# Performance work log

Hardware: AMD Instinct MI355X
Metric: run time of the kernel (lower is better)

Reference implementation:

```python
import jax, jax.numpy as jnp
import numpy as np

V = 256        # vocab (bytes)
DM = 1024      # d_model
NL = 8         # num layers
N = 16         # d_state
K = 4          # d_conv
E = 2 * DM     # d_inner (expand=2)
R = DM // 16   # dt_rank = 64
EPS = 1e-5
B, T = 1, 1024


def setup_inputs() -> dict:
    key = jax.random.key(0)
    ks = jax.random.split(key, 10)
    s = lambda i, shape, scale=0.02: jax.random.normal(ks[i], shape, jnp.float32) * scale
    A_init = jnp.log(jnp.tile(jnp.arange(1, N + 1, dtype=jnp.float32), (NL, E, 1)))
    return {
        "input_ids": jax.random.randint(ks[0], (B, T), 0, V),
        "embed": s(1, (V, DM)),
        "Wxz": s(2, (NL, DM, 2 * E)),            # in_proj (no bias)
        "conv_w": s(3, (NL, E, K), 0.1),          # depthwise causal conv
        "conv_b": jnp.zeros((NL, E), jnp.float32),
        "Wx": s(4, (NL, E, R + 2 * N)),           # x_proj -> dt, B, C
        "Wdt": s(5, (NL, R, E), 0.1),             # dt_proj
        "dt_bias": jnp.full((NL, E), -4.6, jnp.float32),  # softplus(-4.6) ~ 0.01
        "A_log": A_init,                          # A = -exp(A_log), S4D-real init
        "D": jnp.ones((NL, E), jnp.float32),      # skip connection
        "Wout": s(6, (NL, E, DM)),                # out_proj (no bias)
        "norm_w": jnp.ones((NL, DM), jnp.float32),
        "final_norm_w": jnp.ones((DM,), jnp.float32),
        "lm_head_w": s(7, (DM, V)),               # lm_head (no bias)
    }


def rmsnorm(x, w):
    return x * jax.lax.rsqrt(jnp.mean(x * x, axis=-1, keepdims=True) + EPS) * w


def selective_scan(x, dt, A, Bm, Cm, Dp):
    # x, dt: [B,T,E]; A: [E,N]; Bm, Cm: [B,T,N]; Dp: [E]
    dA = jnp.exp(dt[..., None] * A)                              # [B,T,E,N]
    dBx = dt[..., None] * Bm[:, :, None, :] * x[..., None]       # [B,T,E,N]

    def step(h, inp):
        dA_t, dBx_t, C_t = inp                                   # [B,E,N],[B,E,N],[B,N]
        h = dA_t * h + dBx_t
        y = jnp.einsum('ben,bn->be', h, C_t)
        return h, y

    h0 = jnp.zeros((x.shape[0], E, N), x.dtype)
    _, ys = jax.lax.scan(step, h0, (dA.transpose(1, 0, 2, 3),
                                    dBx.transpose(1, 0, 2, 3),
                                    Cm.transpose(1, 0, 2)))
    return ys.transpose(1, 0, 2) + Dp * x                        # [B,T,E]


def mamba_layer(h, p):
    Wxz, cw, cb, Wx, Wdt, dtb, A_log, Dp, Wout, nw = p
    res = h
    u = rmsnorm(h, nw)
    xz = u @ Wxz                                                 # [B,T,2E]
    x, z = jnp.split(xz, 2, axis=-1)
    # causal depthwise conv over time
    xc = jax.lax.conv_general_dilated(x.transpose(0, 2, 1), cw[:, None, :],
                                      (1,), [(K - 1, 0)], feature_group_count=E)
    x = jax.nn.silu(xc.transpose(0, 2, 1) + cb)                  # [B,T,E]
    xdbl = x @ Wx                                                # [B,T,R+2N]
    dt = jax.nn.softplus(xdbl[..., :R] @ Wdt + dtb)              # [B,T,E]
    Bm = xdbl[..., R:R + N]
    Cm = xdbl[..., R + N:]
    A = -jnp.exp(A_log)                                          # [E,N]
    y = selective_scan(x, dt, A, Bm, Cm, Dp)
    y = y * jax.nn.silu(z)
    return res + y @ Wout, None


def reference(input_ids, embed, Wxz, conv_w, conv_b, Wx, Wdt, dt_bias, A_log, D,
              Wout, norm_w, final_norm_w, lm_head_w):
    h = embed[input_ids]                                         # [B,T,DM]
    h, _ = jax.lax.scan(mamba_layer, h,
                        (Wxz, conv_w, conv_b, Wx, Wdt, dt_bias, A_log, D, Wout, norm_w))
    h = rmsnorm(h, final_norm_w)
    return h @ lm_head_w                                         # logits [B,T,V]
```

## Files before the change

### kernel.cpp

```cpp
#include <hip/hip_runtime.h>
#include <hip/hip_bf16.h>

#define DM_   1024
#define NLAY  8
#define NST   16
#define EE    2048
#define E2    4096
#define RNK   64
#define SEQ   1024
#define NXD   96
#define VOC   256
#define EPS_  1e-5f
#define NCH   32
#define CLEN  32
#define NTHR  256

typedef __attribute__((ext_vector_type(8))) short bf16x8;
typedef __attribute__((ext_vector_type(4))) float f32x4;
typedef __hip_bfloat16 bf16;

__device__ __forceinline__ float sigmoidf_(float x){ return 1.f/(1.f+__expf(-x)); }
__device__ __forceinline__ float softplusf_(float x){ return (x>15.f)?x:log1pf(__expf(x)); }
__device__ __forceinline__ short f2bf_s(float x){
  union { bf16 b; short s; } cv; cv.b = __float2bfloat16(x); return cv.s;
}

__device__ __forceinline__ void gld_lds16(const short* g, short* lds_uniform){
  __builtin_amdgcn_global_load_lds(
      (const __attribute__((address_space(1))) unsigned int*)(const void*)g,
      (__attribute__((address_space(3))) unsigned int*)(void*)lds_uniform,
      16, 0, 0);
}

__device__ void t_job(const float* in, bf16* out, int R, int C, int L, char* smem, int gdim){
  float (*tile)[33] = (float(*)[33])smem;
  int tC = C >> 5, tR = R >> 5;
  int per = tC * tR, total = per * L;
  int tx = threadIdx.x & 31, ty = threadIdx.x >> 5;
  for (int it = blockIdx.x; it < total; it += gdim){
    int l = it / per, rem = it - l*per;
    int tc = rem % tC, tr = rem / tC;
    const float* inp = in + (size_t)l*R*C;
    bf16* outp = out + (size_t)l*R*C;
    int c0 = tc*32, r0 = tr*32;
    __syncthreads();
#pragma unroll
    for (int j = 0; j < 4; j++)
      tile[ty + j*8][tx] = inp[(size_t)(r0+ty+j*8)*C + c0+tx];
    __syncthreads();
#pragma unroll
    for (int j = 0; j < 4; j++)
      outp[(size_t)(c0+ty+j*8)*R + r0+tx] = __float2bfloat16(tile[tx][ty+j*8]);
  }
}

__global__ __launch_bounds__(256) void k_prep(
    const float* __restrict__ Wxz, const float* __restrict__ Wout,
    const float* __restrict__ Wx, const float* __restrict__ Wdt,
    const float* __restrict__ lmw,
    bf16* wxz_bf, bf16* wout_bf, bf16* wx_bf, bf16* wdt_bf, bf16* lm_bf){
  __shared__ __align__(16) char smem[4352];
  int gdim = gridDim.x;
  t_job(Wxz,  wxz_bf,  DM_, E2,  NLAY, smem, gdim);
  t_job(Wout, wout_bf, EE,  DM_, NLAY, smem, gdim);
  t_job(Wx,   wx_bf,   EE,  NXD, NLAY, smem, gdim);
  t_job(Wdt,  wdt_bf,  RNK, EE,  NLAY, smem, gdim);
  t_job(lmw,  lm_bf,   DM_, VOC, 1,    smem, gdim);
}

__global__ void k_rmsnorm_fuse(const int* __restrict__ ids, const float* __restrict__ emb,
                               float* __restrict__ h, const float* __restrict__ s0,
                               const float* __restrict__ s1, const float* __restrict__ w,
                               bf16* __restrict__ u, float* __restrict__ zout){
  int t = blockIdx.x;
  float* hp = h + (size_t)t*DM_;
  float v[4];
  float ss = 0.f;
#pragma unroll
  for (int j = 0; j < 4; j++){
    int i = threadIdx.x + j*256;
    float x;
    if (ids){ x = emb[(size_t)ids[t]*DM_ + i]; hp[i] = x; }
    else { x = hp[i] + s0[(size_t)t*DM_ + i] + s1[(size_t)t*DM_ + i]; hp[i] = x; }
    v[j] = x; ss += x*x;
  }
#pragma unroll
  for (int o = 32; o > 0; o >>= 1) ss += __shfl_down(ss, o, 64);
  __shared__ float red[4];
  if ((threadIdx.x & 63) == 0) red[threadIdx.x >> 6] = ss;
  __syncthreads();
  float tot = red[0]+red[1]+red[2]+red[3];
  float sc = rsqrtf(tot*(1.f/DM_) + EPS_);
  bf16* up = u + (size_t)t*DM_;
#pragma unroll
  for (int j = 0; j < 4; j++){
    int i = threadIdx.x + j*256;
    up[i] = __float2bfloat16(v[j]*sc*w[i]);
  }
  if (zout) zout[(size_t)t*VOC + threadIdx.x] = 0.f;
}

template<int BM, int BN, int NWM, int NWN, int MODE>
__global__ __launch_bounds__(256) void k_gemm(
    const short* __restrict__ A, const short* __restrict__ Bt, float* __restrict__ C,
    int M, int N, int K, int Ksplit)
{
  constexpr int BK = 64;
  constexpr int WM = BM/NWM, WN = BN/NWN;
  constexpr int MT = WM/16, NT = WN/16;
  constexpr int ABY = BM*BK*2, BBY = BN*BK*2;
  constexpr int AISS = ABY/4096, BISS = BBY/4096;
  __shared__ __align__(16) short As[2][BM*BK];
  __shared__ __align__(16) short Bs[2][BN*BK];
  int tid = threadIdx.x, lane = tid & 63, wave = tid >> 6;
  int wr = wave / NWN, wc = wave % NWN;
  int m0 = blockIdx.x * BM, n0 = blockIdx.y * BN;
  int lrow = lane & 15, lq = lane >> 4;
  int wbase = (tid & ~63) * 16;

  int kbeg = blockIdx.z * Ksplit;
  int nk = Ksplit / BK;

  f32x4 acc[MT][NT];
#pragma unroll
  for (int i = 0; i < MT; i++)
#pragma unroll
    for (int j = 0; j < NT; j++) acc[i][j] = (f32x4){0.f,0.f,0.f,0.f};

  auto stage = [&](int k0, int buf){
#pragma unroll
    for (int i = 0; i < AISS; i++){
      int off = i*4096 + tid*16;
      int row = off >> 7;
      int kc  = ((off >> 4) & 7) ^ (row & 7);
      gld_lds16(A + (size_t)(m0+row)*K + k0 + kc*8, As[buf] + ((i*4096 + wbase) >> 1));
    }
#pragma unroll
    for (int i = 0; i < BISS; i++){
      int off = i*4096 + tid*16;
      int row = off >> 7;
      int kc  = ((off >> 4) & 7) ^ (row & 7);
      gld_lds16(Bt + (size_t)(n0+row)*K + k0 + kc*8, Bs[buf] + ((i*4096 + wbase) >> 1));
    }
  };

  stage(kbeg, 0);
  __syncthreads();
  for (int it = 0; it < nk; it++){
    int cur = it & 1;
    if (it + 1 < nk) stage(kbeg + (it+1)*BK, cur ^ 1);
#pragma unroll
    for (int s = 0; s < 2; s++){
      bf16x8 af[MT], bfr[NT];
#pragma unroll
      for (int mt = 0; mt < MT; mt++){
        int row = wr*WM + mt*16 + lrow;
        int cc = (s*4 + lq) ^ (row & 7);
        af[mt] = *(const bf16x8*)(As[cur] + row*BK + cc*8);
      }
#pragma unroll
      for (int nt = 0; nt < NT; nt++){
        int row = wc*WN + nt*16 + lrow;
        int cc = (s*4 + lq) ^ (row & 7);
        bfr[nt] = *(const bf16x8*)(Bs[cur] + row*BK + cc*8);
      }
#pragma unroll
      for (int mt = 0; mt < MT; mt++)
#pragma unroll
        for (int nt = 0; nt < NT; nt++)
          acc[mt][nt] = __builtin_amdgcn_mfma_f32_16x16x32_bf16(af[mt], bfr[nt], acc[mt][nt], 0,0,0);
    }
    __syncthreads();
  }

  size_t slab = (MODE == 4) ? (size_t)blockIdx.z * M * N : 0;
#pragma unroll
  for (int mt = 0; mt < MT; mt++){
    int row = m0 + wr*WM + mt*16 + lq*4;
#pragma unroll
    for (int nt = 0; nt < NT; nt++){
      int col = n0 + wc*WN + nt*16 + lrow;
#pragma unroll
      for (int r = 0; r < 4; r++){
        float v = acc[mt][nt][r];
        size_t idx = slab + (size_t)(row + r)*N + col;
        if (MODE == 5) atomicAdd(&C[idx], v);
        else C[idx] = v;
      }
    }
  }
}

__global__ void k_conv_silu(const float* __restrict__ xz, const float* __restrict__ cw,
                            const float* __restrict__ cb, float* __restrict__ xact,
                            bf16* __restrict__ xbf, float* __restrict__ xdbl){
  int t = blockIdx.y;
  int e = blockIdx.x*256 + threadIdx.x;
  float4 w4 = *(const float4*)(cw + (size_t)e*4);
  float acc = cb[e];
  if (t >= 3){
    acc += xz[(size_t)(t-3)*E2 + e]*w4.x + xz[(size_t)(t-2)*E2 + e]*w4.y
         + xz[(size_t)(t-1)*E2 + e]*w4.z + xz[(size_t)t*E2 + e]*w4.w;
  } else {
    const float* wp = (const float*)&w4;
#pragma unroll
    for (int k = 0; k < 4; k++){ int tt = t-3+k; if (tt >= 0) acc += xz[(size_t)tt*E2 + e]*wp[k]; }
  }
  float xv = acc * sigmoidf_(acc);
  size_t id = (size_t)t*EE + e;
  xact[id] = xv;
  xbf[id] = __float2bfloat16(xv);
  if (id < SEQ*NXD) xdbl[id] = 0.f;
}

__global__ __launch_bounds__(256) void k_dt_scanA(
    const float* __restrict__ xdbl, const short* __restrict__ WdtT,
    const float* __restrict__ dtb, const float* __restrict__ Alog,
    const float* __restrict__ xact, float* __restrict__ dtbuf,
    float* __restrict__ S, float* __restrict__ dtsum)
{
  __shared__ __align__(16) char smem[22528];
  short* As = (short*)smem;
  short* Bs = (short*)(smem + 8192);
  float (*dts)[65]  = (float(*)[65])smem;
  float (*Bcol)[17] = (float(*)[17])(smem + 16640);
  int tid = threadIdx.x;
  int lane = tid & 63, wave = tid >> 6;
  int wr = wave >> 1, wc = wave & 1, lrow = lane & 15, lq = lane >> 4;
  int m0 = blockIdx.x*64, n0 = blockIdx.y*64;

  {
    int row = tid >> 2;
    int kq  = (tid & 3) << 4;
    const float* src = xdbl + (size_t)(m0+row)*NXD + kq;
    short tmp[16] __attribute__((aligned(16)));
#pragma unroll
    for (int j = 0; j < 16; j++) tmp[j] = f2bf_s(src[j]);
    int c0 = ((kq>>3) + 0) ^ (row & 7);
    int c1 = ((kq>>3) + 1) ^ (row & 7);
    *(bf16x8*)(As + row*64 + c0*8) = *(const bf16x8*)(tmp);
    *(bf16x8*)(As + row*64 + c1*8) = *(const bf16x8*)(tmp + 8);
  }
  {
    int wbase = (tid & ~63) * 16;
#pragma unroll
    for (int i = 0; i < 2; i++){
      int off = i*4096 + tid*16;
      int row = off >> 7;
      int kc  = ((off >> 4) & 7) ^ (row & 7);
      gld_lds16(WdtT + (size_t)(n0+row)*RNK + kc*8, Bs + ((i*4096 + wbase) >> 1));
    }
  }
  __syncthreads();
  f32x4 acc[2][2];
#pragma unroll
  for (int i = 0; i < 2; i++)
#pragma unroll
    for (int j = 0; j < 2; j++) acc[i][j] = (f32x4){0.f,0.f,0.f,0.f};
#pragma unroll
  for (int s = 0; s < 2; s++){
    bf16x8 af[2], bfr[2];
#pragma unroll
    for (int mt = 0; mt < 2; mt++){
      int row = wr*32 + mt*16 + lrow;
      int cc = (s*4 + lq) ^ (row & 7);
      af[mt] = *(const bf16x8*)(As + row*64 + cc*8);
    }
#pragma unroll
    for (int nt = 0; nt < 2; nt++){
      int row = wc*32 + nt*16 + lrow;
      int cc = (s*4 + lq) ^ (row & 7);
      bfr[nt] = *(const bf16x8*)(Bs + row*64 + cc*8);
    }
#pragma unroll
    for (int mt = 0; mt < 2; mt++)
#pragma unroll
      for (int nt = 0; nt < 2; nt++)
        acc[mt][nt] = __builtin_amdgcn_mfma_f32_16x16x32_bf16(af[mt], bfr[nt], acc[mt][nt], 0,0,0);
  }
  __syncthreads();

#pragma unroll
  for (int mt = 0; mt < 2; mt++){
    int rl = wr*32 + mt*16 + lq*4;
#pragma unroll
    for (int nt = 0; nt < 2; nt++){
      int cl = wc*32 + nt*16 + lrow;
#pragma unroll
      for (int r = 0; r < 4; r++){
        float v = softplusf_(acc[mt][nt][r] + dtb[n0 + cl]);
        dtbuf[(size_t)(m0 + rl + r)*EE + n0 + cl] = v;
        dts[rl + r][cl] = v;
      }
    }
  }
  {
    int row = tid >> 2, n4 = (tid & 3) << 2;
    float4 b4 = *(const float4*)(xdbl + (size_t)(m0+row)*NXD + RNK + n4);
    Bcol[row][n4+0] = b4.x; Bcol[row][n4+1] = b4.y;
    Bcol[row][n4+2] = b4.z; Bcol[row][n4+3] = b4.w;
  }
  __syncthreads();

  if (tid < 128){
    int ch = tid >> 6, el = tid & 63;
    int e = n0 + el;
    int c = (m0 >> 5) + ch;
    int t0 = c*CLEN;
    const float* Al = Alog + (size_t)e*NST;
    float Ae[NST];
#pragma unroll
    for (int n = 0; n < NST; n++) Ae[n] = -__expf(Al[n]);
    float h[NST];
#pragma unroll
    for (int n = 0; n < NST; n++) h[n] = 0.f;
    float ds = 0.f;
    for (int tt = 0; tt < CLEN; tt++){
      float dtv = dts[ch*CLEN + tt][el];
      float xv  = xact[(size_t)(t0+tt)*EE + e];
      ds += dtv;
      float sx = dtv*xv;
#pragma unroll
      for (int n = 0; n < NST; n++)
        h[n] = __expf(dtv*Ae[n])*h[n] + sx*Bcol[ch*CLEN + tt][n];
    }
    float* Sp = S + ((size_t)c*EE + e)*NST;
#pragma unroll
    for (int n = 0; n < NST; n++) Sp[n] = h[n];
    dtsum[(size_t)c*EE + e] = ds;
  }
}

__global__ void k_scanC(const float* __restrict__ dt, const float* __restrict__ x,
                        const float* __restrict__ xdbl, const float* __restrict__ Alog,
                        const float* __restrict__ Dp, const float* __restrict__ S,
                        const float* __restrict__ dtsum, const float* __restrict__ xz,
                        bf16* __restrict__ ybf){
  int e = blockIdx.x*256 + threadIdx.x;
  int c = blockIdx.y;
  int t0 = c*CLEN;
  float Ae[NST];
#pragma unroll
  for (int n = 0; n < NST; n++) Ae[n] = -__expf(Alog[(size_t)e*NST + n]);
  __shared__ float Bsm[CLEN][NST], Csm[CLEN][NST];
  for (int i = threadIdx.x; i < CLEN*NST; i += 256){
    int tt = i>>4, n = i&15;
    Bsm[tt][n] = xdbl[(size_t)(t0+tt)*NXD + RNK + n];
    Csm[tt][n] = xdbl[(size_t)(t0+tt)*NXD + RNK + NST + n];
  }
  __syncthreads();
  float h[NST];
#pragma unroll
  for (int n = 0; n < NST; n++) h[n] = 0.f;
  for (int j = 0; j < c; j++){
    float dsj = dtsum[(size_t)j*EE + e];
    const float* Sj = S + ((size_t)j*EE + e)*NST;
#pragma unroll
    for (int n = 0; n < NST; n++)
      h[n] = __expf(dsj*Ae[n])*h[n] + Sj[n];
  }
  float Dv = Dp[e];
  for (int tt = 0; tt < CLEN; tt++){
    float dtv = dt[(size_t)(t0+tt)*EE + e];
    float xv  = x[(size_t)(t0+tt)*EE + e];
    float sx = dtv*xv;
    float y = Dv*xv;
#pragma unroll
    for (int n = 0; n < NST; n++){
      h[n] = __expf(dtv*Ae[n])*h[n] + sx*Bsm[tt][n];
      y += h[n]*Csm[tt][n];
    }
    float zv = xz[(size_t)(t0+tt)*E2 + EE + e];
    y *= zv*sigmoidf_(zv);
    ybf[(size_t)(t0+tt)*EE + e] = __float2bfloat16(y);
  }
}

extern "C" void kernel_launch(void* const* d_in, const int* in_sizes, int n_in,
                              void* d_out, int out_size, void* d_ws, size_t ws_size,
                              hipStream_t stream)
{
  const int*   ids  = (const int*)d_in[0];
  const float* emb  = (const float*)d_in[1];
  const float* Wxz  = (const float*)d_in[2];
  const float* cw   = (const float*)d_in[3];
  const float* cb   = (const float*)d_in[4];
  const float* Wx   = (const float*)d_in[5];
  const float* Wdt  = (const float*)d_in[6];
  const float* dtb  = (const float*)d_in[7];
  const float* Alog = (const float*)d_in[8];
  const float* Dp   = (const float*)d_in[9];
  const float* Wout = (const float*)d_in[10];
  const float* nw   = (const float*)d_in[11];
  const float* fnw  = (const float*)d_in[12];
  const float* lmw  = (const float*)d_in[13];

  char* p = (char*)d_ws;
  auto alloc = [&](size_t bytes){ void* r = (void*)p; p += (bytes + 255) & ~(size_t)255; return r; };
  bf16* wxz_bf  = (bf16*)alloc((size_t)NLAY*E2*DM_*2);
  bf16* wout_bf = (bf16*)alloc((size_t)NLAY*DM_*EE*2);
  bf16* wx_bf   = (bf16*)alloc((size_t)NLAY*NXD*EE*2);
  bf16* wdt_bf  = (bf16*)alloc((size_t)NLAY*EE*RNK*2);
  bf16* lm_bf   = (bf16*)alloc((size_t)VOC*DM_*2);
  float* h      = (float*)alloc((size_t)SEQ*DM_*4);
  float* hslab  = (float*)alloc((size_t)2*SEQ*DM_*4);
  bf16* u_bf    = (bf16*)alloc((size_t)SEQ*DM_*2);
  float* xzb    = (float*)alloc((size_t)SEQ*E2*4);
  float* xact   = (float*)alloc((size_t)SEQ*EE*4);
  bf16* x_bf    = (bf16*)alloc((size_t)SEQ*EE*2);
  float* xdbl   = (float*)alloc((size_t)SEQ*NXD*4);
  float* dtbuf  = (float*)alloc((size_t)SEQ*EE*4);
  float* Sbuf   = (float*)alloc((size_t)NCH*EE*NST*4);
  float* dtsum  = (float*)alloc((size_t)NCH*EE*4);
  bf16* y_bf    = (bf16*)alloc((size_t)SEQ*EE*2);

  k_prep<<<512, 256, 0, stream>>>(Wxz, Wout, Wx, Wdt, lmw,
                                  wxz_bf, wout_bf, wx_bf, wdt_bf, lm_bf);

  for (int l = 0; l < NLAY; l++){
    k_rmsnorm_fuse<<<SEQ, 256, 0, stream>>>(
        l == 0 ? ids : nullptr, emb, h,
        hslab, hslab + (size_t)SEQ*DM_,
        nw + (size_t)l*DM_, u_bf, nullptr);
    k_gemm<128,64,2,2,0><<<dim3(SEQ/128, E2/64, 1), 256, 0, stream>>>(
        (const short*)u_bf, (const short*)(wxz_bf + (size_t)l*E2*DM_), xzb,
        SEQ, E2, DM_, DM_);
    k_conv_silu<<<dim3(EE/256, SEQ), 256, 0, stream>>>(
        xzb, cw + (size_t)l*EE*4, cb + (size_t)l*EE, xact, x_bf, xdbl);
    k_gemm<32,96,2,2,5><<<dim3(SEQ/32, 1, 16), 256, 0, stream>>>(
        (const short*)x_bf, (const short*)(wx_bf + (size_t)l*NXD*EE), xdbl,
        SEQ, NXD, EE, EE/16);
    k_dt_scanA<<<dim3(SEQ/64, EE/64), 256, 0, stream>>>(
        xdbl, (const short*)(wdt_bf + (size_t)l*EE*RNK), dtb + (size_t)l*EE,
        Alog + (size_t)l*EE*NST, xact, dtbuf, Sbuf, dtsum);
    k_scanC<<<dim3(EE/256, NCH), 256, 0, stream>>>(
        dtbuf, xact, xdbl, Alog + (size_t)l*EE*NST, Dp + (size_t)l*EE,
        Sbuf, dtsum, xzb, y_bf);
    k_gemm<64,64,2,2,4><<<dim3(SEQ/64, DM_/64, 2), 256, 0, stream>>>(
        (const short*)y_bf, (const short*)(wout_bf + (size_t)l*DM_*EE), hslab,
        SEQ, DM_, EE, EE/2);
  }
  k_rmsnorm_fuse<<<SEQ, 256, 0, stream>>>(
      nullptr, emb, h, hslab, hslab + (size_t)SEQ*DM_, fnw, u_bf, (float*)d_out);
  k_gemm<64,64,2,2,5><<<dim3(SEQ/64, VOC/64, 4), 256, 0, stream>>>(
      (const short*)u_bf, (const short*)lm_bf, (float*)d_out,
      SEQ, VOC, DM_, DM_/4);
}
```

Baseline: 1.237 ms.

## Fuse causal conv+SiLU into x_proj GEMM and vectorize weight transpose

Replaces the separate conv+SiLU kernel and the x_proj split-K GEMM with one kernel that computes the conv and SiLU while staging the A tile into LDS. This removes the bf16 x buffer round trip and one launch per layer. Zeroing of xdbl moves into the rmsnorm kernel. The weight prep transpose now uses float4 loads, 64-row tiles, 16-byte stores and a larger grid. The conv work is done inside GEMM staging with scalar strided loads, which may be less coalesced than the old elementwise kernel.

```diff
diff --git a/kernel.cpp b/kernel.cpp
--- a/kernel.cpp
+++ b/kernel.cpp
@@ -13,9 +13,9 @@
 #define EPS_  1e-5f
 #define NCH   32
 #define CLEN  32
-#define NTHR  256
 
 typedef __attribute__((ext_vector_type(8))) short bf16x8;
+typedef __attribute__((ext_vector_type(8))) unsigned short u16x8;
 typedef __attribute__((ext_vector_type(4))) float f32x4;
 typedef __hip_bfloat16 bf16;
 
@@ -32,25 +32,32 @@
       16, 0, 0);
 }
 
-__device__ void t_job(const float* in, bf16* out, int R, int C, int L, char* smem, int gdim){
-  float (*tile)[33] = (float(*)[33])smem;
-  int tC = C >> 5, tR = R >> 5;
+__device__ void t_job(const float* in, bf16* out, int R, int C, int L,
+                      short* tileT , int gdim){
+  int tC = C >> 5, tR = R >> 6;
   int per = tC * tR, total = per * L;
-  int tx = threadIdx.x & 31, ty = threadIdx.x >> 5;
+  int tid = threadIdx.x;
+  int cc = tid >> 3, sg = tid & 7;
   for (int it = blockIdx.x; it < total; it += gdim){
     int l = it / per, rem = it - l*per;
     int tc = rem % tC, tr = rem / tC;
     const float* inp = in + (size_t)l*R*C;
     bf16* outp = out + (size_t)l*R*C;
-    int c0 = tc*32, r0 = tr*32;
+    int c0 = tc*32, r0 = tr*64;
     __syncthreads();
 #pragma unroll
-    for (int j = 0; j < 4; j++)
-      tile[ty + j*8][tx] = inp[(size_t)(r0+ty+j*8)*C + c0+tx];
+    for (int jr = 0; jr < 2; jr++){
+      int idx = tid + jr*256;
+      int row = idx >> 3, fc = idx & 7;
+      float4 v = *(const float4*)(inp + (size_t)(r0+row)*C + c0 + fc*4);
+      tileT[(fc*4+0)*68 + row] = f2bf_s(v.x);
+      tileT[(fc*4+1)*68 + row] = f2bf_s(v.y);
+      tileT[(fc*4+2)*68 + row] = f2bf_s(v.z);
+      tileT[(fc*4+3)*68 + row] = f2bf_s(v.w);
+    }
     __syncthreads();
-#pragma unroll
-    for (int j = 0; j < 4; j++)
-      outp[(size_t)(c0+ty+j*8)*R + r0+tx] = __float2bfloat16(tile[tx][ty+j*8]);
+    u16x8 o = *(const u16x8*)(tileT + cc*68 + sg*8);
+    *(u16x8*)((unsigned short*)outp + (size_t)(c0+cc)*R + r0 + sg*8) = o;
   }
 }
 
@@ -59,19 +66,20 @@
     const float* __restrict__ Wx, const float* __restrict__ Wdt,
     const float* __restrict__ lmw,
     bf16* wxz_bf, bf16* wout_bf, bf16* wx_bf, bf16* wdt_bf, bf16* lm_bf){
-  __shared__ __align__(16) char smem[4352];
+  __shared__ __align__(16) short tileT[32*68];
   int gdim = gridDim.x;
-  t_job(Wxz,  wxz_bf,  DM_, E2,  NLAY, smem, gdim);
-  t_job(Wout, wout_bf, EE,  DM_, NLAY, smem, gdim);
-  t_job(Wx,   wx_bf,   EE,  NXD, NLAY, smem, gdim);
-  t_job(Wdt,  wdt_bf,  RNK, EE,  NLAY, smem, gdim);
-  t_job(lmw,  lm_bf,   DM_, VOC, 1,    smem, gdim);
+  t_job(Wxz,  wxz_bf,  DM_, E2,  NLAY, tileT, gdim);
+  t_job(Wout, wout_bf, EE,  DM_, NLAY, tileT, gdim);
+  t_job(Wx,   wx_bf,   EE,  NXD, NLAY, tileT, gdim);
+  t_job(Wdt,  wdt_bf,  RNK, EE,  NLAY, tileT, gdim);
+  t_job(lmw,  lm_bf,   DM_, VOC, 1,    tileT, gdim);
 }
 
 __global__ void k_rmsnorm_fuse(const int* __restrict__ ids, const float* __restrict__ emb,
                                float* __restrict__ h, const float* __restrict__ s0,
                                const float* __restrict__ s1, const float* __restrict__ w,
-                               bf16* __restrict__ u, float* __restrict__ zout){
+                               bf16* __restrict__ u, float* __restrict__ xdz,
+                               float* __restrict__ zout){
   int t = blockIdx.x;
   float* hp = h + (size_t)t*DM_;
   float v[4];
@@ -97,6 +105,7 @@
     int i = threadIdx.x + j*256;
     up[i] = __float2bfloat16(v[j]*sc*w[i]);
   }
+  if (xdz && threadIdx.x < NXD) xdz[(size_t)t*NXD + threadIdx.x] = 0.f;
   if (zout) zout[(size_t)t*VOC + threadIdx.x] = 0.f;
 }
 
@@ -191,26 +200,91 @@
   }
 }
 
-__global__ void k_conv_silu(const float* __restrict__ xz, const float* __restrict__ cw,
-                            const float* __restrict__ cb, float* __restrict__ xact,
-                            bf16* __restrict__ xbf, float* __restrict__ xdbl){
-  int t = blockIdx.y;
-  int e = blockIdx.x*256 + threadIdx.x;
-  float4 w4 = *(const float4*)(cw + (size_t)e*4);
-  float acc = cb[e];
-  if (t >= 3){
-    acc += xz[(size_t)(t-3)*E2 + e]*w4.x + xz[(size_t)(t-2)*E2 + e]*w4.y
-         + xz[(size_t)(t-1)*E2 + e]*w4.z + xz[(size_t)t*E2 + e]*w4.w;
-  } else {
-    const float* wp = (const float*)&w4;
-#pragma unroll
-    for (int k = 0; k < 4; k++){ int tt = t-3+k; if (tt >= 0) acc += xz[(size_t)tt*E2 + e]*wp[k]; }
-  }
-  float xv = acc * sigmoidf_(acc);
-  size_t id = (size_t)t*EE + e;
-  xact[id] = xv;
-  xbf[id] = __float2bfloat16(xv);
-  if (id < SEQ*NXD) xdbl[id] = 0.f;
+__global__ __launch_bounds__(256) void k_wx_conv(
+    const float* __restrict__ xzb, const float* __restrict__ cw, const float* __restrict__ cb,
+    const short* __restrict__ WxT, float* __restrict__ xact, float* __restrict__ xdbl)
+{
+  __shared__ __align__(16) short As[2][32*64];
+  __shared__ __align__(16) short Bs[2][96*64];
+  int tid = threadIdx.x, lane = tid & 63, wave = tid >> 6;
+  int wr = wave >> 1, wc = wave & 1;
+  int lrow = lane & 15, lq = lane >> 4;
+  int wbase = (tid & ~63) * 16;
+  int m0 = blockIdx.x * 32;
+  int kbeg = blockIdx.z * 128;
+
+  int arow = tid >> 3;
+  int ag   = tid & 7;
+  int t    = m0 + arow;
+
+  auto stageA = [&](int k0, int buf){
+    int e0 = k0 + ag*8;
+    float v[8];
+#pragma unroll
+    for (int j = 0; j < 8; j++){
+      int e = e0 + j;
+      float4 w4 = *(const float4*)(cw + (size_t)e*4);
+      float a = cb[e];
+      if (t >= 3){
+        a += xzb[(size_t)(t-3)*E2 + e]*w4.x + xzb[(size_t)(t-2)*E2 + e]*w4.y
+           + xzb[(size_t)(t-1)*E2 + e]*w4.z + xzb[(size_t)t*E2 + e]*w4.w;
+      } else {
+        const float* wp = (const float*)&w4;
+#pragma unroll
+        for (int k = 0; k < 4; k++){ int tt = t-3+k; if (tt >= 0) a += xzb[(size_t)tt*E2 + e]*wp[k]; }
+      }
+      v[j] = a * sigmoidf_(a);
+    }
+    float4 v0 = {v[0],v[1],v[2],v[3]}, v1 = {v[4],v[5],v[6],v[7]};
+    *(float4*)(xact + (size_t)t*EE + e0)     = v0;
+    *(float4*)(xact + (size_t)t*EE + e0 + 4) = v1;
+    short tmp[8] __attribute__((aligned(16)));
+#pragma unroll
+    for (int j = 0; j < 8; j++) tmp[j] = f2bf_s(v[j]);
+    int c = ag ^ (arow & 7);
+    *(bf16x8*)(As[buf] + arow*64 + c*8) = *(const bf16x8*)tmp;
+  };
+  auto stageB = [&](int k0, int buf){
+#pragma unroll
+    for (int i = 0; i < 3; i++){
+      int off = i*4096 + tid*16;
+      int row = off >> 7;
+      int kc  = ((off >> 4) & 7) ^ (row & 7);
+      gld_lds16(WxT + (size_t)row*EE + k0 + kc*8, Bs[buf] + ((i*4096 + wbase) >> 1));
+    }
+  };
+
+  stageA(kbeg, 0); stageB(kbeg, 0);
+  __syncthreads();
+  f32x4 acc[3];
+#pragma unroll
+  for (int j = 0; j < 3; j++) acc[j] = (f32x4){0.f,0.f,0.f,0.f};
+  for (int it = 0; it < 2; it++){
+    int cur = it & 1;
+    if (it == 0){ stageA(kbeg + 64, 1); stageB(kbeg + 64, 1); }
+#pragma unroll
+    for (int s = 0; s < 2; s++){
+      int rowa = wr*16 + lrow;
+      int cca = (s*4 + lq) ^ (rowa & 7);
+      bf16x8 af = *(const bf16x8*)(As[cur] + rowa*64 + cca*8);
+#pragma unroll
+      for (int nt = 0; nt < 3; nt++){
+        int rowb = wc*48 + nt*16 + lrow;
+        int ccb = (s*4 + lq) ^ (rowb & 7);
+        bf16x8 bfr = *(const bf16x8*)(Bs[cur] + rowb*64 + ccb*8);
+        acc[nt] = __builtin_amdgcn_mfma_f32_16x16x32_bf16(af, bfr, acc[nt], 0,0,0);
+      }
+    }
+    __syncthreads();
+  }
+  int rowg = m0 + wr*16 + lq*4;
+#pragma unroll
+  for (int nt = 0; nt < 3; nt++){
+    int col = wc*48 + nt*16 + lrow;
+#pragma unroll
+    for (int r = 0; r < 4; r++)
+      atomicAdd(&xdbl[(size_t)(rowg+r)*NXD + col], acc[nt][r]);
+  }
 }
 
 __global__ __launch_bounds__(256) void k_dt_scanA(
@@ -407,29 +481,26 @@
   bf16* u_bf    = (bf16*)alloc((size_t)SEQ*DM_*2);
   float* xzb    = (float*)alloc((size_t)SEQ*E2*4);
   float* xact   = (float*)alloc((size_t)SEQ*EE*4);
-  bf16* x_bf    = (bf16*)alloc((size_t)SEQ*EE*2);
   float* xdbl   = (float*)alloc((size_t)SEQ*NXD*4);
   float* dtbuf  = (float*)alloc((size_t)SEQ*EE*4);
   float* Sbuf   = (float*)alloc((size_t)NCH*EE*NST*4);
   float* dtsum  = (float*)alloc((size_t)NCH*EE*4);
   bf16* y_bf    = (bf16*)alloc((size_t)SEQ*EE*2);
 
-  k_prep<<<512, 256, 0, stream>>>(Wxz, Wout, Wx, Wdt, lmw,
-                                  wxz_bf, wout_bf, wx_bf, wdt_bf, lm_bf);
+  k_prep<<<2048, 256, 0, stream>>>(Wxz, Wout, Wx, Wdt, lmw,
+                                   wxz_bf, wout_bf, wx_bf, wdt_bf, lm_bf);
 
   for (int l = 0; l < NLAY; l++){
     k_rmsnorm_fuse<<<SEQ, 256, 0, stream>>>(
         l == 0 ? ids : nullptr, emb, h,
         hslab, hslab + (size_t)SEQ*DM_,
-        nw + (size_t)l*DM_, u_bf, nullptr);
+        nw + (size_t)l*DM_, u_bf, xdbl, nullptr);
     k_gemm<128,64,2,2,0><<<dim3(SEQ/128, E2/64, 1), 256, 0, stream>>>(
         (const short*)u_bf, (const short*)(wxz_bf + (size_t)l*E2*DM_), xzb,
         SEQ, E2, DM_, DM_);
-    k_conv_silu<<<dim3(EE/256, SEQ), 256, 0, stream>>>(
-        xzb, cw + (size_t)l*EE*4, cb + (size_t)l*EE, xact, x_bf, xdbl);
-    k_gemm<32,96,2,2,5><<<dim3(SEQ/32, 1, 16), 256, 0, stream>>>(
-        (const short*)x_bf, (const short*)(wx_bf + (size_t)l*NXD*EE), xdbl,
-        SEQ, NXD, EE, EE/16);
+    k_wx_conv<<<dim3(SEQ/32, 1, 16), 256, 0, stream>>>(
+        xzb, cw + (size_t)l*EE*4, cb + (size_t)l*EE,
+        (const short*)(wx_bf + (size_t)l*NXD*EE), xact, xdbl);
     k_dt_scanA<<<dim3(SEQ/64, EE/64), 256, 0, stream>>>(
         xdbl, (const short*)(wdt_bf + (size_t)l*EE*RNK), dtb + (size_t)l*EE,
         Alog + (size_t)l*EE*NST, xact, dtbuf, Sbuf, dtsum);
@@ -441,7 +512,7 @@
         SEQ, DM_, EE, EE/2);
   }
   k_rmsnorm_fuse<<<SEQ, 256, 0, stream>>>(
-      nullptr, emb, h, hslab, hslab + (size_t)SEQ*DM_, fnw, u_bf, (float*)d_out);
+      nullptr, emb, h, hslab, hslab + (size_t)SEQ*DM_, fnw, u_bf, nullptr, (float*)d_out);
   k_gemm<64,64,2,2,5><<<dim3(SEQ/64, VOC/64, 4), 256, 0, stream>>>(
       (const short*)u_bf, (const short*)lm_bf, (float*)d_out,
       SEQ, VOC, DM_, DM_/4);
```

Result: slower. 1.339 ms (+8.3%).
